# Kernel optimization log

Measured on AMD Instinct MI355X. Metric: run time of the kernel, lower is better.

Reference implementation:

```python
import jax, jax.numpy as jnp
import numpy as np
import math

B, L, D, H = 2, 1024, 1024, 16
HD = D // H          # 64
FFN = 2 * D          # 2048 (dim << 1 default)
TEMP = math.sqrt(HD)
EPS = 1e-5


def _layer_norm(x, g, b):
    m = jnp.mean(x, axis=-1, keepdims=True)
    v = jnp.mean(jnp.square(x - m), axis=-1, keepdims=True)
    return (x - m) * jax.lax.rsqrt(v + EPS) * g + b


def setup_inputs() -> dict:
    key = jax.random.key(0)
    ks = jax.random.split(key, 16)
    s = 0.02
    return {
        "x": jax.random.normal(ks[0], (B, L, D), jnp.float32),
        "edge_bias": jax.random.normal(ks[1], (B, L, L, H), jnp.float32),
        "padding_mask": jnp.zeros((B, L), dtype=bool),
        "wq": jax.random.normal(ks[2], (D, D), jnp.float32) * s,
        "wk": jax.random.normal(ks[3], (D, D), jnp.float32) * s,
        "wv": jax.random.normal(ks[4], (D, D), jnp.float32) * s,
        "wo": jax.random.normal(ks[5], (D, D), jnp.float32) * s,
        "bo": jnp.zeros((D,), jnp.float32),
        "wg": jax.random.normal(ks[6], (D, D), jnp.float32) * s,
        "bg": jnp.zeros((D,), jnp.float32),
        "w1": jax.random.normal(ks[7], (D, FFN), jnp.float32) * s,
        "b1": jnp.zeros((FFN,), jnp.float32),
        "w2": jax.random.normal(ks[8], (FFN, D), jnp.float32) * s,
        "b2": jnp.zeros((D,), jnp.float32),
        "ln1_g": jnp.ones((D,), jnp.float32),
        "ln1_b": jnp.zeros((D,), jnp.float32),
        "ln2_g": jnp.ones((D,), jnp.float32),
        "ln2_b": jnp.zeros((D,), jnp.float32),
    }


def reference(x, edge_bias, padding_mask, wq, wk, wv, wo, bo, wg, bg,
              w1, b1, w2, b2, ln1_g, ln1_b, ln2_g, ln2_b):
    # --- BiasedAttention (q = k = v = x) ---
    qh = (x @ wq).reshape(B, L, H, HD) / TEMP   # bqhd
    kh = (x @ wk).reshape(B, L, H, HD)          # bkhd
    vh = (x @ wv).reshape(B, L, H, HD)          # bkhd
    # scores in 'bkqh' layout, matching torch einsum('bqhd,bkhd->bkqh')
    attn = jnp.einsum('bqhd,bkhd->bkqh', qh, kh)
    attn = attn + jnp.transpose(edge_bias, (0, 2, 1, 3))  # bias is [b,q,k,h] -> [b,k,q,h]
    # key padding mask: masks entire key rows (axis 1 in bkqh)
    attn = jnp.where(padding_mask[:, :, None, None], -jnp.inf, attn)
    attn = jax.nn.softmax(attn, axis=1)  # softmax over keys
    o = jnp.einsum('bkqh,bkhd->bqhd', attn, vh).reshape(B, L, D)
    o = jax.nn.sigmoid(x @ wg + bg) * o          # sigmoid gate from raw q
    delta_x = o @ wo + bo
    attn_out = jnp.transpose(attn, (0, 2, 1, 3))  # [b,q,k,h]
    # --- residual + LN + FFN (eval mode: dropout/DropPath are identity) ---
    x = _layer_norm(x + delta_x, ln1_g, ln1_b)
    ffn = jax.nn.silu(x @ w1 + b1) @ w2 + b2
    x = _layer_norm(x + ffn, ln2_g, ln2_b)
    return (x, attn_out)
```

## Files before the change

kernel.cpp:

```cpp
#include <hip/hip_runtime.h>

typedef __bf16 bf16;
typedef _Float16 f16;
typedef bf16 bf16x8 __attribute__((ext_vector_type(8)));
typedef bf16 bf16x4 __attribute__((ext_vector_type(4)));
typedef f16 f16x4 __attribute__((ext_vector_type(4)));
typedef float f32x4 __attribute__((ext_vector_type(4)));


__global__ __launch_bounds__(256) void kprep(
    const float* __restrict__ x, bf16* __restrict__ xbf,
    const float* __restrict__ wq, const float* __restrict__ wk, const float* __restrict__ wv,
    const float* __restrict__ wg, const float* __restrict__ wo, const float* __restrict__ w1,
    const float* __restrict__ w2, bf16* __restrict__ wqT, bf16* __restrict__ wkT,
    bf16* __restrict__ wvT, bf16* __restrict__ wgT, bf16* __restrict__ woT,
    bf16* __restrict__ w1T, bf16* __restrict__ w2T) {
  int bid = blockIdx.x;
  int tid = threadIdx.x;

  if (bid >= 9216) {
    int i = (bid - 9216) * 256 + tid;
    f32x4 v = *(const f32x4*)(x + (long)i * 4);
    bf16x4 o;
#pragma unroll
    for (int j = 0; j < 4; j++) o[j] = (bf16)v[j];
    *(bf16x4*)(xbf + (long)i * 4) = o;
    return;
  }

  __shared__ float t[32][33];
  const float* src;
  bf16* dst;
  int R, C, tile;
  if (bid < 5120) {
    int seg = bid >> 10;
    tile = bid & 1023;
    R = 1024; C = 1024;
    if (seg == 0) { src = wq; dst = wqT; }
    else if (seg == 1) { src = wk; dst = wkT; }
    else if (seg == 2) { src = wv; dst = wvT; }
    else if (seg == 3) { src = wg; dst = wgT; }
    else { src = wo; dst = woT; }
  } else if (bid < 7168) {
    tile = bid - 5120; R = 1024; C = 2048; src = w1; dst = w1T;
  } else {
    tile = bid - 7168; R = 2048; C = 1024; src = w2; dst = w2T;
  }
  int txs = (C == 2048) ? 6 : 5;
  int c0 = (tile & ((1 << txs) - 1)) << 5, r0 = (tile >> txs) << 5;
  int tx = tid & 31, ty = tid >> 5;
#pragma unroll
  for (int i = 0; i < 32; i += 8)
    t[ty + i][tx] = src[(long)(r0 + ty + i) * C + c0 + tx];
  __syncthreads();
#pragma unroll
  for (int i = 0; i < 32; i += 8)
    dst[(long)(c0 + ty + i) * R + r0 + tx] = (bf16)t[tx][ty + i];
}

static constexpr int MODE_QK = 0;
static constexpr int MODE_VT = 1;
static constexpr int MODE_G = 2;
static constexpr int MODE_SCOREF16 = 3;
static constexpr int MODE_SCORE_SC = 4;
static constexpr int MODE_PV = 5;
static constexpr int MODE_PV_SLOW = 6;
static constexpr int MODE_WO = 7;
static constexpr int MODE_FFN1 = 8;
static constexpr int MODE_FFN2 = 9;
static constexpr int MODE_QKVG = 10;

template <int MODE>
__global__ __launch_bounds__(256) void gemm_bt(
    const void* __restrict__ Av, const bf16* __restrict__ Bt, void* __restrict__ Out,
    const float* __restrict__ bias, const float* __restrict__ gate,
    int M, int N, int K, int lda, int ldb, long sA, long sB, float alpha) {
  const int z = blockIdx.z;
  const bf16* A = (const bf16*)Av + (long)z * sA;
  Bt += (long)z * sB;
  const int bb = z >> 4, hh = z & 15;

  __shared__ bf16 As[128][40];
  __shared__ bf16 Bs[128][40];

  const int tid = threadIdx.x;
  const int m0 = blockIdx.y * 128, n0 = blockIdx.x * 128;
  const int lane = tid & 63, wave = tid >> 6;
  const int wm = (wave >> 1) * 64, wn = (wave & 1) * 64;
  const int l15 = lane & 15, quad = lane >> 4;

  f32x4 acc[4][4] = {};

  for (int k0 = 0; k0 < K; k0 += 32) {
    bf16x8 av[2], bv[2];
#pragma unroll
    for (int u = 0; u < 2; u++) {
      int c = tid + u * 256;
      int row = c >> 2, kc = (c & 3) << 3;
      if (MODE == MODE_PV_SLOW) {
        const float* Af = (const float*)Av;
        long rb = ((long)bb << 24) + hh + ((long)(m0 + row) << 14) + ((long)(k0 + kc) << 4);
#pragma unroll
        for (int j = 0; j < 8; j++) av[u][j] = (bf16)Af[rb + j * 16];
      } else {
        av[u] = *(const bf16x8*)(A + (long)(m0 + row) * lda + (k0 + kc));
      }
      int brow = n0 + row;
      if (brow < N) {
        bv[u] = *(const bf16x8*)(Bt + (long)brow * ldb + (k0 + kc));
      } else {
#pragma unroll
        for (int j = 0; j < 8; j++) bv[u][j] = (bf16)0.0f;
      }
    }
    __syncthreads();
#pragma unroll
    for (int u = 0; u < 2; u++) {
      int c = tid + u * 256;
      int row = c >> 2, kc = (c & 3) << 3;
      *(bf16x8*)&As[row][kc] = av[u];
      *(bf16x8*)&Bs[row][kc] = bv[u];
    }
    __syncthreads();

    bf16x8 af[4], bfr[4];
#pragma unroll
    for (int t = 0; t < 4; t++) {
      af[t] = *(const bf16x8*)&As[wm + t * 16 + l15][quad << 3];
      bfr[t] = *(const bf16x8*)&Bs[wn + t * 16 + l15][quad << 3];
    }
#pragma unroll
    for (int mt = 0; mt < 4; mt++)
#pragma unroll
      for (int nt = 0; nt < 4; nt++)
        acc[mt][nt] =
            __builtin_amdgcn_mfma_f32_16x16x32_bf16(af[mt], bfr[nt], acc[mt][nt], 0, 0, 0);
  }

#pragma unroll
  for (int mt = 0; mt < 4; mt++) {
#pragma unroll
    for (int nt = 0; nt < 4; nt++) {
#pragma unroll
      for (int r = 0; r < 4; r++) {
        int m = m0 + wm + mt * 16 + (quad << 2) + r;
        int n = n0 + wn + nt * 16 + l15;
        if (n >= N) continue;
        float v = acc[mt][nt][r] * alpha;
        if (MODE == MODE_QK) {
          long off = ((long)((m >> 10) * 16 + (n >> 6)) * 1024 + (m & 1023)) * 64 + (n & 63);
          ((bf16*)Out)[off] = (bf16)v;
        } else if (MODE == MODE_VT) {
          long off = ((long)((m >> 10) * 16 + (n >> 6)) * 64 + (n & 63)) * 1024 + (m & 1023);
          ((bf16*)Out)[off] = (bf16)v;
        } else if (MODE == MODE_G) {
          float t = v + bias[n];
          ((float*)Out)[(long)m * N + n] = 1.0f / (1.0f + __expf(-t));
        } else if (MODE == MODE_QKVG) {
          int sec = n >> 10, nn = n & 1023;
          bf16* ob = (bf16*)Out;
          if (sec == 0) {
            long off = ((long)((m >> 10) * 16 + (nn >> 6)) * 1024 + (m & 1023)) * 64 + (nn & 63);
            ob[off] = (bf16)(v * 0.125f);
          } else if (sec == 1) {
            long off = ((long)((m >> 10) * 16 + (nn >> 6)) * 1024 + (m & 1023)) * 64 + (nn & 63);
            (ob + 2097152)[off] = (bf16)v;
          } else if (sec == 2) {
            long off = ((long)((m >> 10) * 16 + (nn >> 6)) * 64 + (nn & 63)) * 1024 + (m & 1023);
            (ob + 4194304)[off] = (bf16)v;
          } else {
            float t = v + bias[nn];
            ((float*)(ob + 6291456))[(long)m * 1024 + nn] = 1.0f / (1.0f + __expf(-t));
          }
        } else if (MODE == MODE_SCOREF16) {
          ((f16*)Out)[((long)z << 20) + ((long)m << 10) + n] = (f16)v;
        } else if (MODE == MODE_SCORE_SC) {
          long off = ((long)bb << 24) + ((long)m << 14) + ((long)n << 4) + hh;
          ((float*)Out)[off] = v;
        } else if (MODE == MODE_PV || MODE == MODE_PV_SLOW) {
          long off = ((long)(bb * 1024 + m)) * 1024 + hh * 64 + n;
          ((bf16*)Out)[off] = (bf16)(v * gate[off]);
        } else if (MODE == MODE_WO) {
          ((float*)Out)[(long)m * N + n] = v + bias[n];
        } else if (MODE == MODE_FFN1) {
          float t = v + bias[n];
          ((bf16*)Out)[(long)m * N + n] = (bf16)(t / (1.0f + __expf(-t)));
        } else {
          ((float*)Out)[(long)m * N + n] = v + bias[n];
        }
      }
    }
  }
}

__global__ __launch_bounds__(256) void attn_softmax16(float* __restrict__ attnf,
                                                      void* __restrict__ Sf,
                                                      const float* __restrict__ ebias,
                                                      const unsigned char* __restrict__ mask) {
  __shared__ float sm[16][1028];
  __shared__ float invs[16];
  int bx = blockIdx.x;
  int q = bx & 1023, b = bx >> 10;
  int tid = threadIdx.x;
  int lane = tid & 63, wave = tid >> 6;
  long sbase = ((long)b << 24) + ((long)q << 14);

  const f16* S = (const f16*)Sf;
#pragma unroll
  for (int h = 0; h < 16; h++) {
    long rb = (((long)((b << 4) + h) << 10) + q) << 10;
    f16x4 v = *(const f16x4*)(S + rb + tid * 4);
    f32x4 f;
#pragma unroll
    for (int j = 0; j < 4; j++) f[j] = (float)v[j];
    *(f32x4*)&sm[h][tid * 4] = f;
  }
  __syncthreads();

#pragma unroll
  for (int it = 0; it < 16; it++) {
    int j = tid + it * 256;
    int k = j >> 2, c = (j & 3) << 2;
    f32x4 e = *(const f32x4*)(ebias + sbase + ((long)k << 4) + c);
#pragma unroll
    for (int jj = 0; jj < 4; jj++) sm[c + jj][k] += e[jj];
  }
  __syncthreads();

  for (int k = tid; k < 1024; k += 256) {
    if (mask[(b << 10) + k]) {
#pragma unroll
      for (int h = 0; h < 16; h++) sm[h][k] = -1e30f;
    }
  }
  __syncthreads();

  for (int h = wave * 4; h < wave * 4 + 4; h++) {
    float mx = -1e30f;
    for (int k = lane; k < 1024; k += 64) mx = fmaxf(mx, sm[h][k]);
#pragma unroll
    for (int d = 32; d; d >>= 1) mx = fmaxf(mx, __shfl_xor(mx, d, 64));
    float sum = 0.f;
    for (int k = lane; k < 1024; k += 64) {
      float p = __expf(sm[h][k] - mx);
      sm[h][k] = p;
      sum += p;
    }
#pragma unroll
    for (int d = 32; d; d >>= 1) sum += __shfl_xor(sum, d, 64);
    if (lane == 0) invs[h] = 1.0f / sum;
  }
  __syncthreads();

#pragma unroll
  for (int it = 0; it < 16; it++) {
    int j = tid + it * 256;
    int k = j >> 2, c = (j & 3) << 2;
    f32x4 v;
#pragma unroll
    for (int jj = 0; jj < 4; jj++) v[jj] = sm[c + jj][k] * invs[c + jj];
    *(f32x4*)(attnf + sbase + ((long)k << 4) + c) = v;
  }
#pragma unroll
  for (int h = 0; h < 16; h++) {
    long rb = (((long)((b << 4) + h) << 10) + q) << 10;
    float inv = invs[h];
    f32x4 f = *(const f32x4*)&sm[h][tid * 4];
    bf16x4 o;
#pragma unroll
    for (int j = 0; j < 4; j++) o[j] = (bf16)(f[j] * inv);
    *(bf16x4*)((bf16*)Sf + rb + tid * 4) = o;
  }
}

template <int FAST>
__global__ __launch_bounds__(256) void attn_softmax(float* __restrict__ attnf,
                                                    void* __restrict__ Sf,
                                                    const float* __restrict__ ebias,
                                                    const unsigned char* __restrict__ mask) {
  __shared__ float sm[8][1028];
  int bx = blockIdx.x;
  int hb = (bx & 1) * 8;
  int q = (bx >> 1) & 1023;
  int b = bx >> 11;
  int tid = threadIdx.x;
  int lane = tid & 63, wave = tid >> 6;
  long sbase = ((long)b << 24) + ((long)q << 14) + hb;

  for (int i = tid; i < 2048; i += 256) {
    int k = i >> 1, c = (i & 1) * 4;
    long off = sbase + ((long)k << 4) + c;
    f32x4 s = *(const f32x4*)(attnf + off);
    f32x4 e = *(const f32x4*)(ebias + off);
#pragma unroll
    for (int j = 0; j < 4; j++) sm[c + j][k] = s[j] + e[j];
  }
  __syncthreads();

  for (int k = tid; k < 1024; k += 256) {
    if (mask[(b << 10) + k]) {
#pragma unroll
      for (int h = 0; h < 8; h++) sm[h][k] = -1e30f;
    }
  }
  __syncthreads();

  for (int h = wave * 2; h < wave * 2 + 2; h++) {
    float mx = -1e30f;
    for (int k = lane; k < 1024; k += 64) mx = fmaxf(mx, sm[h][k]);
#pragma unroll
    for (int d = 32; d; d >>= 1) mx = fmaxf(mx, __shfl_xor(mx, d, 64));
    float sum = 0.f;
    for (int k = lane; k < 1024; k += 64) {
      float p = __expf(sm[h][k] - mx);
      sm[h][k] = p;
      sum += p;
    }
#pragma unroll
    for (int d = 32; d; d >>= 1) sum += __shfl_xor(sum, d, 64);
    float inv = 1.0f / sum;
    for (int k = lane; k < 1024; k += 64) sm[h][k] *= inv;
  }
  __syncthreads();

  for (int i = tid; i < 2048; i += 256) {
    int k = i >> 1, c = (i & 1) * 4;
    f32x4 v;
#pragma unroll
    for (int j = 0; j < 4; j++) v[j] = sm[c + j][k];
    *(f32x4*)(attnf + sbase + ((long)k << 4) + c) = v;
  }
}

template <int MODE>
__global__ __launch_bounds__(256) void layernorm_k(
    const float* __restrict__ a32, const float* __restrict__ b32, const float* __restrict__ g,
    const float* __restrict__ be, float* __restrict__ of32, bf16* __restrict__ obf) {
  __shared__ float red[8];
  long base = (long)blockIdx.x << 10;
  int tid = threadIdx.x;
  int lane = tid & 63, wave = tid >> 6;
  float h[4], sum = 0.f, sq = 0.f;
#pragma unroll
  for (int t = 0; t < 4; t++) {
    int i = tid + t * 256;
    float v = a32[base + i] + b32[base + i];
    h[t] = v;
    sum += v;
    sq += v * v;
  }
#pragma unroll
  for (int d = 32; d; d >>= 1) {
    sum += __shfl_xor(sum, d, 64);
    sq += __shfl_xor(sq, d, 64);
  }
  if (lane == 0) { red[wave] = sum; red[4 + wave] = sq; }
  __syncthreads();
  sum = red[0] + red[1] + red[2] + red[3];
  sq = red[4] + red[5] + red[6] + red[7];
  float mean = sum * (1.0f / 1024.0f);
  float var = sq * (1.0f / 1024.0f) - mean * mean;
  float rstd = rsqrtf(var + 1e-5f);
#pragma unroll
  for (int t = 0; t < 4; t++) {
    int i = tid + t * 256;
    float o = (h[t] - mean) * rstd * g[i] + be[i];
    of32[base + i] = o;
    if (MODE == 0) obf[base + i] = (bf16)o;
  }
}

extern "C" void kernel_launch(void* const* d_in, const int* in_sizes, int n_in, void* d_out,
                              int out_size, void* d_ws, size_t ws_size, hipStream_t stream) {
  const float* x = (const float*)d_in[0];
  const float* ebias = (const float*)d_in[1];
  const unsigned char* pmask = (const unsigned char*)d_in[2];
  const float* wq = (const float*)d_in[3];
  const float* wk = (const float*)d_in[4];
  const float* wv = (const float*)d_in[5];
  const float* wo = (const float*)d_in[6];
  const float* bo = (const float*)d_in[7];
  const float* wg = (const float*)d_in[8];
  const float* bg = (const float*)d_in[9];
  const float* w1 = (const float*)d_in[10];
  const float* b1 = (const float*)d_in[11];
  const float* w2 = (const float*)d_in[12];
  const float* b2 = (const float*)d_in[13];
  const float* ln1g = (const float*)d_in[14];
  const float* ln1b = (const float*)d_in[15];
  const float* ln2g = (const float*)d_in[16];
  const float* ln2b = (const float*)d_in[17];

  char* p = (char*)d_ws;
  bf16* xbf = (bf16*)p;  p += 4194304;
  bf16* wqT = (bf16*)p;  p += 2097152;
  bf16* wkT = (bf16*)p;  p += 2097152;
  bf16* wvT = (bf16*)p;  p += 2097152;
  bf16* wgT = (bf16*)p;  p += 2097152;
  bf16* woT = (bf16*)p;  p += 2097152;
  bf16* w1T = (bf16*)p;  p += 4194304;
  bf16* w2T = (bf16*)p;  p += 4194304;
  bf16* qws = (bf16*)p;  p += 4194304;
  bf16* kws = (bf16*)p;  p += 4194304;
  bf16* vtws = (bf16*)p; p += 4194304;
  float* gws = (float*)p; p += 8388608;
  bf16* ows = (bf16*)p;  p += 4194304;
  float* delta = (float*)p; p += 8388608;
  bf16* x1bf = (bf16*)p; p += 4194304;
  float* x1f = (float*)p; p += 8388608;
  bf16* ffn1 = (bf16*)p; p += 8388608;
  float* ffn2 = (float*)p; p += 8388608;
  size_t base_used = (size_t)(p - (char*)d_ws);
  void* Pws = (void*)p;
  bool fast = (base_used + 67108864ull) <= ws_size;
  (void)kws;

  float* xout = (float*)d_out;
  float* attnf = (float*)d_out + 2097152;

  dim3 blk(256);

  kprep<<<11264, blk, 0, stream>>>(x, xbf, wq, wk, wv, wg, wo, w1, w2, wqT, wkT, wvT, wgT, woT,
                                   w1T, w2T);

  gemm_bt<MODE_QKVG><<<dim3(32, 16, 1), blk, 0, stream>>>(xbf, wqT, qws, bg, nullptr, 2048, 4096,
                                                          1024, 1024, 1024, 0, 0, 1.0f);

  if (fast) {
    gemm_bt<MODE_SCOREF16><<<dim3(8, 8, 32), blk, 0, stream>>>(
        qws, kws, Pws, nullptr, nullptr, 1024, 1024, 64, 64, 64, 65536, 65536, 1.0f);
    attn_softmax16<<<2048, blk, 0, stream>>>(attnf, Pws, ebias, pmask);
    gemm_bt<MODE_PV><<<dim3(1, 8, 32), blk, 0, stream>>>((bf16*)Pws, vtws, ows, nullptr, gws,
                                                         1024, 64, 1024, 1024, 1024, 1048576,
                                                         65536, 1.0f);
  } else {
    gemm_bt<MODE_SCORE_SC><<<dim3(8, 8, 32), blk, 0, stream>>>(
        qws, kws, attnf, nullptr, nullptr, 1024, 1024, 64, 64, 64, 65536, 65536, 1.0f);
    attn_softmax<0><<<4096, blk, 0, stream>>>(attnf, nullptr, ebias, pmask);
    gemm_bt<MODE_PV_SLOW><<<dim3(1, 8, 32), blk, 0, stream>>>(attnf, vtws, ows, nullptr, gws,
                                                              1024, 64, 1024, 1024, 1024, 0,
                                                              65536, 1.0f);
  }

  gemm_bt<MODE_WO><<<dim3(8, 16, 1), blk, 0, stream>>>(ows, woT, delta, bo, nullptr, 2048, 1024,
                                                       1024, 1024, 1024, 0, 0, 1.0f);
  layernorm_k<0><<<2048, blk, 0, stream>>>(x, delta, ln1g, ln1b, x1f, x1bf);
  gemm_bt<MODE_FFN1><<<dim3(16, 16, 1), blk, 0, stream>>>(x1bf, w1T, ffn1, b1, nullptr, 2048,
                                                          2048, 1024, 1024, 1024, 0, 0, 1.0f);
  gemm_bt<MODE_FFN2><<<dim3(8, 16, 1), blk, 0, stream>>>(ffn1, w2T, ffn2, b2, nullptr, 2048, 1024,
                                                         2048, 2048, 2048, 0, 0, 1.0f);
  layernorm_k<1><<<2048, blk, 0, stream>>>(x1f, ffn2, ln2g, ln2b, xout, nullptr);
}
```

Measured before the change: 572.9 us.

## Restructure edge-bias softmax to use fp16 LDS and register-resident rows

The 16-head softmax kernel now stages edge bias (with the padding mask folded in) into an fp16 shared buffer instead of fp32 scores. Score rows are held in registers per wave, and normalized probabilities are written once in bf16 to global and in fp16 back to LDS for the transposed fp32 output. This halves LDS usage to allow more resident blocks, removes several barriers and passes, and drops the separate rescale loops. In exchange, the fp32 attention output now carries fp16 rounding of the probabilities, and edge-bias loads become scalar.

```diff
diff --git a/kernel.cpp b/kernel.cpp
--- a/kernel.cpp
+++ b/kernel.cpp
@@ -5,6 +5,7 @@
 typedef bf16 bf16x8 __attribute__((ext_vector_type(8)));
 typedef bf16 bf16x4 __attribute__((ext_vector_type(4)));
 typedef f16 f16x4 __attribute__((ext_vector_type(4)));
+typedef f16 f16x8 __attribute__((ext_vector_type(8)));
 typedef float f32x4 __attribute__((ext_vector_type(4)));
 
 
@@ -193,62 +194,86 @@
   }
 }
 
-__global__ __launch_bounds__(256) void attn_softmax16(float* __restrict__ attnf,
-                                                      void* __restrict__ Sf,
-                                                      const float* __restrict__ ebias,
-                                                      const unsigned char* __restrict__ mask) {
-  __shared__ float sm[16][1028];
-  __shared__ float invs[16];
+__global__ __launch_bounds__(256, 4) void attn_softmax16(float* __restrict__ attnf,
+                                                         void* __restrict__ Sf,
+                                                         const float* __restrict__ ebias,
+                                                         const unsigned char* __restrict__ mask) {
+  __shared__ f16 sm[16][1032];
   int bx = blockIdx.x;
   int q = bx & 1023, b = bx >> 10;
   int tid = threadIdx.x;
   int lane = tid & 63, wave = tid >> 6;
   long sbase = ((long)b << 24) + ((long)q << 14);
 
-  const f16* S = (const f16*)Sf;
-#pragma unroll
-  for (int h = 0; h < 16; h++) {
-    long rb = (((long)((b << 4) + h) << 10) + q) << 10;
-    f16x4 v = *(const f16x4*)(S + rb + tid * 4);
-    f32x4 f;
-#pragma unroll
-    for (int j = 0; j < 4; j++) f[j] = (float)v[j];
-    *(f32x4*)&sm[h][tid * 4] = f;
-  }
-  __syncthreads();
-
-#pragma unroll
-  for (int it = 0; it < 16; it++) {
-    int j = tid + it * 256;
-    int k = j >> 2, c = (j & 3) << 2;
-    f32x4 e = *(const f32x4*)(ebias + sbase + ((long)k << 4) + c);
-#pragma unroll
-    for (int jj = 0; jj < 4; jj++) sm[c + jj][k] += e[jj];
-  }
-  __syncthreads();
-
-  for (int k = tid; k < 1024; k += 256) {
-    if (mask[(b << 10) + k]) {
-#pragma unroll
-      for (int h = 0; h < 16; h++) sm[h][k] = -1e30f;
-    }
-  }
-  __syncthreads();
-
-  for (int h = wave * 4; h < wave * 4 + 4; h++) {
-    float mx = -1e30f;
-    for (int k = lane; k < 1024; k += 64) mx = fmaxf(mx, sm[h][k]);
+  {
+    int h = tid & 15;
+    int kb = (tid >> 4) << 4;
+#pragma unroll
+    for (int it = 0; it < 4; it++) {
+      int k0 = kb + it * 256;
+      unsigned mw[4];
+      *(uint4*)mw = *(const uint4*)(mask + (b << 10) + k0);
+      f16 hv[16];
+#pragma unroll
+      for (int i = 0; i < 16; i++) {
+        float v = ebias[sbase + (long)(k0 + i) * 16 + h];
+        bool msk = (mw[i >> 2] >> ((i & 3) * 8)) & 255;
+        hv[i] = msk ? (f16)(-60000.0f) : (f16)v;
+      }
+      *(f16x8*)&sm[h][k0] = *(f16x8*)&hv[0];
+      *(f16x8*)&sm[h][k0 + 8] = *(f16x8*)&hv[8];
+    }
+  }
+
+  f16* S = (f16*)Sf;
+  f16x8 sv[4][2];
+#pragma unroll
+  for (int hi = 0; hi < 4; hi++) {
+    int h = wave * 4 + hi;
+    long srow = (((long)((b << 4) + h) << 10) + q) << 10;
+    sv[hi][0] = *(const f16x8*)(S + srow + lane * 8);
+    sv[hi][1] = *(const f16x8*)(S + srow + lane * 8 + 512);
+  }
+  __syncthreads();
+
+#pragma unroll
+  for (int hi = 0; hi < 4; hi++) {
+    int h = wave * 4 + hi;
+    long srow = (((long)((b << 4) + h) << 10) + q) << 10;
+    f16x8 bv0 = *(const f16x8*)&sm[h][lane * 8];
+    f16x8 bv1 = *(const f16x8*)&sm[h][lane * 8 + 512];
+    float s_[16];
+#pragma unroll
+    for (int j = 0; j < 8; j++) {
+      s_[j] = (float)sv[hi][0][j] + (float)bv0[j];
+      s_[8 + j] = (float)sv[hi][1][j] + (float)bv1[j];
+    }
+    float mx = s_[0];
+#pragma unroll
+    for (int j = 1; j < 16; j++) mx = fmaxf(mx, s_[j]);
 #pragma unroll
     for (int d = 32; d; d >>= 1) mx = fmaxf(mx, __shfl_xor(mx, d, 64));
     float sum = 0.f;
-    for (int k = lane; k < 1024; k += 64) {
-      float p = __expf(sm[h][k] - mx);
-      sm[h][k] = p;
-      sum += p;
+#pragma unroll
+    for (int j = 0; j < 16; j++) {
+      s_[j] = __expf(s_[j] - mx);
+      sum += s_[j];
     }
 #pragma unroll
     for (int d = 32; d; d >>= 1) sum += __shfl_xor(sum, d, 64);
-    if (lane == 0) invs[h] = 1.0f / sum;
+    float inv = 1.0f / sum;
+    bf16x8 pb0, pb1;
+    f16 ph[16];
+#pragma unroll
+    for (int j = 0; j < 16; j++) {
+      float pv = s_[j] * inv;
+      ph[j] = (f16)pv;
+      if (j < 8) pb0[j] = (bf16)pv; else pb1[j - 8] = (bf16)pv;
+    }
+    *(bf16x8*)((bf16*)Sf + srow + lane * 8) = pb0;
+    *(bf16x8*)((bf16*)Sf + srow + lane * 8 + 512) = pb1;
+    *(f16x8*)&sm[h][lane * 8] = *(f16x8*)&ph[0];
+    *(f16x8*)&sm[h][lane * 8 + 512] = *(f16x8*)&ph[8];
   }
   __syncthreads();
 
@@ -258,18 +283,8 @@
     int k = j >> 2, c = (j & 3) << 2;
     f32x4 v;
 #pragma unroll
-    for (int jj = 0; jj < 4; jj++) v[jj] = sm[c + jj][k] * invs[c + jj];
+    for (int jj = 0; jj < 4; jj++) v[jj] = (float)sm[c + jj][k];
     *(f32x4*)(attnf + sbase + ((long)k << 4) + c) = v;
-  }
-#pragma unroll
-  for (int h = 0; h < 16; h++) {
-    long rb = (((long)((b << 4) + h) << 10) + q) << 10;
-    float inv = invs[h];
-    f32x4 f = *(const f32x4*)&sm[h][tid * 4];
-    bf16x4 o;
-#pragma unroll
-    for (int j = 0; j < 4; j++) o[j] = (bf16)(f[j] * inv);
-    *(bf16x4*)((bf16*)Sf + rb + tid * 4) = o;
   }
 }
 
```

Measured after the change: 559.5 us. -2.3%, faster.
